# Kernel optimization log

Measured on AMD Instinct MI355X. Metric: run time of the kernel, lower is better.

Reference implementation:

```python
import jax, jax.numpy as jnp
import numpy as np

SEQ_LEN = 96
PRED_LEN = 16
HIDDEN = 64
FEAT = 7
BATCH = 512


def setup_inputs() -> dict:
    key = jax.random.key(0)
    ks = jax.random.split(key, 7)
    s = 1.0 / np.sqrt(HIDDEN)  # PyTorch LSTM/Linear default uniform init bound
    x = jax.random.normal(ks[0], (BATCH, SEQ_LEN, FEAT), jnp.float32)
    W_ih = jax.random.uniform(ks[1], (4 * HIDDEN, FEAT), jnp.float32, -s, s)
    W_hh = jax.random.uniform(ks[2], (4 * HIDDEN, HIDDEN), jnp.float32, -s, s)
    b_ih = jax.random.uniform(ks[3], (4 * HIDDEN,), jnp.float32, -s, s)
    b_hh = jax.random.uniform(ks[4], (4 * HIDDEN,), jnp.float32, -s, s)
    fc_W = jax.random.uniform(ks[5], (FEAT, HIDDEN), jnp.float32, -s, s)
    fc_b = jax.random.uniform(ks[6], (FEAT,), jnp.float32, -s, s)
    return {"x": x, "W_ih": W_ih, "W_hh": W_hh, "b_ih": b_ih, "b_hh": b_hh,
            "fc_W": fc_W, "fc_b": fc_b}


def _lstm_last(x, h, c, W_ih, W_hh, b):
    # Precompute input-to-gate projections for the whole window: [B, T, 4H]
    xg = jnp.einsum('bti,gi->btg', x, W_ih) + b

    def cell(carry, xg_t):
        h, c = carry
        gates = xg_t + h @ W_hh.T            # [B, 4H], PyTorch gate order i,f,g,o
        i, f, g, o = jnp.split(gates, 4, axis=-1)
        i = jax.nn.sigmoid(i)
        f = jax.nn.sigmoid(f)
        g = jnp.tanh(g)
        o = jax.nn.sigmoid(o)
        c = f * c + i * g
        h = o * jnp.tanh(c)
        return (h, c), None

    (h, c), _ = jax.lax.scan(cell, (h, c), jnp.swapaxes(xg, 0, 1))
    return h, c


def reference(x, W_ih, W_hh, b_ih, b_hh, fc_W, fc_b):
    B = x.shape[0]
    b = b_ih + b_hh
    h = jnp.zeros((B, HIDDEN), x.dtype)
    c = jnp.zeros((B, HIDDEN), x.dtype)
    outs = []
    for _ in range(PRED_LEN):
        h, c = _lstm_last(x, h, c, W_ih, W_hh, b)
        pred = h @ fc_W.T + fc_b             # [B, 7]
        outs.append(pred)
        x = jnp.concatenate([x[:, 1:, :], pred[:, None, :]], axis=1)
    return jnp.stack(outs, axis=1)           # [B, PRED_LEN, 7]
```

## Files before the change

### kernel.cpp

```cpp
#include <hip/hip_runtime.h>

#define SEQ_LEN 96
#define PRED_LEN 16
#define HIDDEN 64
#define FEAT 7
#define BATCH 512
#define TL (SEQ_LEN + PRED_LEN)
#define XSTR 8

typedef float v2f __attribute__((ext_vector_type(2)));

#define L2E 1.4426950408889634f

__device__ __forceinline__ float qp_xor1(float v) {
    return __int_as_float(__builtin_amdgcn_mov_dpp(__float_as_int(v), 0xB1, 0xF, 0xF, true));
}
__device__ __forceinline__ float qp_xor2(float v) {
    return __int_as_float(__builtin_amdgcn_mov_dpp(__float_as_int(v), 0x4E, 0xF, 0xF, true));
}
__device__ __forceinline__ float qp_rot1(float v) {
    return __int_as_float(__builtin_amdgcn_mov_dpp(__float_as_int(v), 0x39, 0xF, 0xF, true));
}
__device__ __forceinline__ float qp_rot3(float v) {
    return __int_as_float(__builtin_amdgcn_mov_dpp(__float_as_int(v), 0x93, 0xF, 0xF, true));
}

__device__ __forceinline__ v2f pk_mul(v2f a, v2f b) {
    v2f d;
    asm("v_pk_mul_f32 %0, %1, %2" : "=v"(d) : "v"(a), "v"(b));
    return d;
}
__device__ __forceinline__ void pk_fma(v2f& acc, v2f a, v2f b) {
    asm("v_pk_fma_f32 %0, %1, %2, %0" : "+v"(acc) : "v"(a), "v"(b));
}

__global__ __launch_bounds__(256)
__attribute__((amdgpu_waves_per_eu(2, 2)))
void lstm_ar_kernel(
    const float* __restrict__ x,
    const float* __restrict__ W_ih,
    const float* __restrict__ W_hh,
    const float* __restrict__ b_ih,
    const float* __restrict__ b_hh,
    const float* __restrict__ fc_W,
    const float* __restrict__ fc_b,
    float* __restrict__ out)
{
    __shared__ float xs[TL * XSTR];
    __shared__ float hb0[HIDDEN];
    __shared__ float hb1[HIDDEN];
    __shared__ float hscr[HIDDEN];
    __shared__ float fcw[FEAT * HIDDEN];
    __shared__ float fcb[FEAT];

    const int tid = threadIdx.x;
    const int b   = blockIdx.x;
    const int u   = tid >> 2;
    const int q   = tid & 3;

    v2f wh[4][8];
    #pragma unroll
    for (int k = 0; k < 4; ++k) {
        const int gate = (q + k) & 3;
        const float* wr = W_hh + ((gate << 6) + u) * HIDDEN + (q << 4);
        #pragma unroll
        for (int j = 0; j < 8; ++j) wh[k][j] = *(const v2f*)(wr + 2 * j);
    }
    v2f wx[4];
    #pragma unroll
    for (int k = 0; k < 4; ++k) {
        const int gate = (q + k) & 3;
        const int row  = (gate << 6) + u;
        const int c0 = (q << 1), c1 = c0 + 1;
        wx[k].x = W_ih[row * FEAT + c0];
        wx[k].y = (c1 < FEAT) ? W_ih[row * FEAT + c1]
                              : (b_ih[row] + b_hh[row]);
    }

    const float bk  = (q == 2) ? (-2.0f * L2E) : (-L2E);
    const float bm  = (q == 2) ? 2.0f : 1.0f;
    const float bbc = (q == 2) ? -1.0f : 0.0f;

    float* const sink = hscr + ((u + (q << 4)) & 63);
    float* const wa1 = (q == 0) ? (hb1 + u) : sink;
    float* const wa0 = (q == 0) ? (hb0 + u) : sink;

    const float4* const h40 = (const float4*)(hb0 + (q << 4));
    const float4* const h41 = (const float4*)(hb1 + (q << 4));
    const float* const xq = xs + (q << 1);

    for (int i = tid; i < TL * XSTR; i += 256) {
        int r = i >> 3, f = i & 7;
        float v = 1.0f;
        if (f < FEAT) v = (r < SEQ_LEN) ? x[b * SEQ_LEN * FEAT + r * FEAT + f] : 0.0f;
        xs[i] = v;
    }
    for (int i = tid; i < FEAT * HIDDEN; i += 256) fcw[i] = fc_W[i];
    if (tid < FEAT)   fcb[tid] = fc_b[tid];
    if (tid < HIDDEN) hb0[tid] = 0.0f;
    float c = 0.0f;
    __syncthreads();

    auto step = [&](v2f xv, int nrow, const float4* __restrict__ h4,
                    float* __restrict__ wa) -> v2f {
        v2f A0 = pk_mul(wx[0], xv);
        v2f A1 = pk_mul(wx[1], xv);
        v2f A2 = pk_mul(wx[2], xv);
        v2f A3 = pk_mul(wx[3], xv);

        #pragma unroll
        for (int j = 0; j < 4; ++j) {
            float4 hv = h4[j];
            v2f lo; lo.x = hv.x; lo.y = hv.y;
            v2f hi; hi.x = hv.z; hi.y = hv.w;
            pk_fma(A0, wh[0][2*j],   lo);
            pk_fma(A1, wh[1][2*j],   lo);
            pk_fma(A2, wh[2][2*j],   lo);
            pk_fma(A3, wh[3][2*j],   lo);
            pk_fma(A0, wh[0][2*j+1], hi);
            pk_fma(A1, wh[1][2*j+1], hi);
            pk_fma(A2, wh[2][2*j+1], hi);
            pk_fma(A3, wh[3][2*j+1], hi);
        }

        float r0 = A0.x + A0.y;
        float r1 = A1.x + A1.y;
        float r2 = A2.x + A2.y;
        float r3 = A3.x + A3.y;
        float sum = r0 + qp_rot1(r3);
        sum += qp_xor2(r2);
        sum += qp_rot3(r1);

        float e   = __builtin_amdgcn_exp2f(sum * bk);
        float rc  = __builtin_amdgcn_rcpf(1.0f + e);
        float a   = fmaf(bm, rc, bbc);

        float p1 = qp_xor1(a);
        float p2 = qp_xor2(a);
        float p3 = qp_xor2(p1);

        c = fmaf(p1, c, a * p2);
        float e2 = __builtin_amdgcn_exp2f(c * (-2.0f * L2E));
        float rr = __builtin_amdgcn_rcpf(1.0f + e2);
        float th = fmaf(2.0f, rr, -1.0f);
        *wa = p3 * th;

        v2f nxt = *(const v2f*)(xq + nrow * XSTR);
        __syncthreads();
        return nxt;
    };

    for (int k = 0; k < PRED_LEN; ++k) {
        v2f cur = *(const v2f*)(xq + k * XSTR);
        for (int t = 0; t < SEQ_LEN; t += 2) {
            cur = step(cur, k + t + 1, h40, wa1);
            cur = step(cur, k + t + 2, h41, wa0);
        }

        if (tid < FEAT) {
            float p0 = fcb[tid], p1 = 0.0f, p2 = 0.0f, p3 = 0.0f;
            const float4* hh = (const float4*)hb0;
            #pragma unroll
            for (int j = 0; j < 16; ++j) {
                float4 hv = hh[j];
                p0 = fmaf(fcw[tid * HIDDEN + 4 * j + 0], hv.x, p0);
                p1 = fmaf(fcw[tid * HIDDEN + 4 * j + 1], hv.y, p1);
                p2 = fmaf(fcw[tid * HIDDEN + 4 * j + 2], hv.z, p2);
                p3 = fmaf(fcw[tid * HIDDEN + 4 * j + 3], hv.w, p3);
            }
            float pred = (p0 + p1) + (p2 + p3);
            out[(b * PRED_LEN + k) * FEAT + tid] = pred;
            xs[(SEQ_LEN + k) * XSTR + tid] = pred;
        }
        __syncthreads();
    }
}

extern "C" void kernel_launch(void* const* d_in, const int* in_sizes, int n_in,
                              void* d_out, int out_size, void* d_ws, size_t ws_size,
                              hipStream_t stream) {
    const float* x    = (const float*)d_in[0];
    const float* W_ih = (const float*)d_in[1];
    const float* W_hh = (const float*)d_in[2];
    const float* b_ih = (const float*)d_in[3];
    const float* b_hh = (const float*)d_in[4];
    const float* fc_W = (const float*)d_in[5];
    const float* fc_b = (const float*)d_in[6];
    float* out = (float*)d_out;

    lstm_ar_kernel<<<BATCH, 256, 0, stream>>>(x, W_ih, W_hh, b_ih, b_hh, fc_W, fc_b, out);
}
```

Measured before the change: 556.3 us.

## Process two batch rows per block to interleave independent LSTM recurrences

Each block now runs two batch elements in lockstep with one set of register-resident weights. The two independent dependency chains are interleaved, so FMA, transcendental and DPP latency can overlap and the per-step barrier is shared across two rows. The grid is halved to 256 blocks and waves-per-EU is lowered to 1, which gives more registers but leaves fewer waves per CU and fewer blocks than before on a 256-CU part.

```diff
diff --git a/kernel.cpp b/kernel.cpp
--- a/kernel.cpp
+++ b/kernel.cpp
@@ -34,8 +34,10 @@
     asm("v_pk_fma_f32 %0, %1, %2, %0" : "+v"(acc) : "v"(a), "v"(b));
 }
 
+struct VV { v2f a, b; };
+
 __global__ __launch_bounds__(256)
-__attribute__((amdgpu_waves_per_eu(2, 2)))
+__attribute__((amdgpu_waves_per_eu(1, 1)))
 void lstm_ar_kernel(
     const float* __restrict__ x,
     const float* __restrict__ W_ih,
@@ -46,15 +48,17 @@
     const float* __restrict__ fc_b,
     float* __restrict__ out)
 {
-    __shared__ float xs[TL * XSTR];
-    __shared__ float hb0[HIDDEN];
-    __shared__ float hb1[HIDDEN];
+    __shared__ float xsA[TL * XSTR];
+    __shared__ float xsB[TL * XSTR];
+    __shared__ float hA0[HIDDEN], hA1[HIDDEN];
+    __shared__ float hB0[HIDDEN], hB1[HIDDEN];
     __shared__ float hscr[HIDDEN];
     __shared__ float fcw[FEAT * HIDDEN];
     __shared__ float fcb[FEAT];
 
     const int tid = threadIdx.x;
-    const int b   = blockIdx.x;
+    const int bA  = blockIdx.x * 2;
+    const int bB  = bA + 1;
     const int u   = tid >> 2;
     const int q   = tid & 3;
 
@@ -82,95 +86,125 @@
     const float bbc = (q == 2) ? -1.0f : 0.0f;
 
     float* const sink = hscr + ((u + (q << 4)) & 63);
-    float* const wa1 = (q == 0) ? (hb1 + u) : sink;
-    float* const wa0 = (q == 0) ? (hb0 + u) : sink;
-
-    const float4* const h40 = (const float4*)(hb0 + (q << 4));
-    const float4* const h41 = (const float4*)(hb1 + (q << 4));
-    const float* const xq = xs + (q << 1);
+    float* const waA1 = (q == 0) ? (hA1 + u) : sink;
+    float* const waA0 = (q == 0) ? (hA0 + u) : sink;
+    float* const waB1 = (q == 0) ? (hB1 + u) : sink;
+    float* const waB0 = (q == 0) ? (hB0 + u) : sink;
+
+    const float4* const hA40 = (const float4*)(hA0 + (q << 4));
+    const float4* const hA41 = (const float4*)(hA1 + (q << 4));
+    const float4* const hB40 = (const float4*)(hB0 + (q << 4));
+    const float4* const hB41 = (const float4*)(hB1 + (q << 4));
+    const float* const xqA = xsA + (q << 1);
+    const float* const xqB = xsB + (q << 1);
 
     for (int i = tid; i < TL * XSTR; i += 256) {
         int r = i >> 3, f = i & 7;
-        float v = 1.0f;
-        if (f < FEAT) v = (r < SEQ_LEN) ? x[b * SEQ_LEN * FEAT + r * FEAT + f] : 0.0f;
-        xs[i] = v;
+        float vA = 1.0f, vB = 1.0f;
+        if (f < FEAT) {
+            vA = (r < SEQ_LEN) ? x[bA * SEQ_LEN * FEAT + r * FEAT + f] : 0.0f;
+            vB = (r < SEQ_LEN) ? x[bB * SEQ_LEN * FEAT + r * FEAT + f] : 0.0f;
+        }
+        xsA[i] = vA;
+        xsB[i] = vB;
     }
     for (int i = tid; i < FEAT * HIDDEN; i += 256) fcw[i] = fc_W[i];
     if (tid < FEAT)   fcb[tid] = fc_b[tid];
-    if (tid < HIDDEN) hb0[tid] = 0.0f;
-    float c = 0.0f;
+    if (tid < HIDDEN) { hA0[tid] = 0.0f; hB0[tid] = 0.0f; }
+    float cA = 0.0f, cB = 0.0f;
     __syncthreads();
 
-    auto step = [&](v2f xv, int nrow, const float4* __restrict__ h4,
-                    float* __restrict__ wa) -> v2f {
-        v2f A0 = pk_mul(wx[0], xv);
-        v2f A1 = pk_mul(wx[1], xv);
-        v2f A2 = pk_mul(wx[2], xv);
-        v2f A3 = pk_mul(wx[3], xv);
+    auto step = [&](v2f xvA, v2f xvB, int nrow,
+                    const float4* __restrict__ h4A, const float4* __restrict__ h4B,
+                    float* __restrict__ wA, float* __restrict__ wB) -> VV {
+        v2f nA = *(const v2f*)(xqA + nrow * XSTR);
+        v2f nB = *(const v2f*)(xqB + nrow * XSTR);
+
+        v2f A0 = pk_mul(wx[0], xvA);  v2f B0 = pk_mul(wx[0], xvB);
+        v2f A1 = pk_mul(wx[1], xvA);  v2f B1 = pk_mul(wx[1], xvB);
+        v2f A2 = pk_mul(wx[2], xvA);  v2f B2 = pk_mul(wx[2], xvB);
+        v2f A3 = pk_mul(wx[3], xvA);  v2f B3 = pk_mul(wx[3], xvB);
 
         #pragma unroll
         for (int j = 0; j < 4; ++j) {
-            float4 hv = h4[j];
-            v2f lo; lo.x = hv.x; lo.y = hv.y;
-            v2f hi; hi.x = hv.z; hi.y = hv.w;
-            pk_fma(A0, wh[0][2*j],   lo);
-            pk_fma(A1, wh[1][2*j],   lo);
-            pk_fma(A2, wh[2][2*j],   lo);
-            pk_fma(A3, wh[3][2*j],   lo);
-            pk_fma(A0, wh[0][2*j+1], hi);
-            pk_fma(A1, wh[1][2*j+1], hi);
-            pk_fma(A2, wh[2][2*j+1], hi);
-            pk_fma(A3, wh[3][2*j+1], hi);
-        }
-
-        float r0 = A0.x + A0.y;
-        float r1 = A1.x + A1.y;
-        float r2 = A2.x + A2.y;
-        float r3 = A3.x + A3.y;
-        float sum = r0 + qp_rot1(r3);
-        sum += qp_xor2(r2);
-        sum += qp_rot3(r1);
-
-        float e   = __builtin_amdgcn_exp2f(sum * bk);
-        float rc  = __builtin_amdgcn_rcpf(1.0f + e);
-        float a   = fmaf(bm, rc, bbc);
-
-        float p1 = qp_xor1(a);
-        float p2 = qp_xor2(a);
-        float p3 = qp_xor2(p1);
-
-        c = fmaf(p1, c, a * p2);
-        float e2 = __builtin_amdgcn_exp2f(c * (-2.0f * L2E));
-        float rr = __builtin_amdgcn_rcpf(1.0f + e2);
-        float th = fmaf(2.0f, rr, -1.0f);
-        *wa = p3 * th;
-
-        v2f nxt = *(const v2f*)(xq + nrow * XSTR);
+            float4 hvA = h4A[j];
+            float4 hvB = h4B[j];
+            v2f alo; alo.x = hvA.x; alo.y = hvA.y;
+            v2f ahi; ahi.x = hvA.z; ahi.y = hvA.w;
+            v2f blo; blo.x = hvB.x; blo.y = hvB.y;
+            v2f bhi; bhi.x = hvB.z; bhi.y = hvB.w;
+            pk_fma(A0, wh[0][2*j],   alo);  pk_fma(B0, wh[0][2*j],   blo);
+            pk_fma(A1, wh[1][2*j],   alo);  pk_fma(B1, wh[1][2*j],   blo);
+            pk_fma(A2, wh[2][2*j],   alo);  pk_fma(B2, wh[2][2*j],   blo);
+            pk_fma(A3, wh[3][2*j],   alo);  pk_fma(B3, wh[3][2*j],   blo);
+            pk_fma(A0, wh[0][2*j+1], ahi);  pk_fma(B0, wh[0][2*j+1], bhi);
+            pk_fma(A1, wh[1][2*j+1], ahi);  pk_fma(B1, wh[1][2*j+1], bhi);
+            pk_fma(A2, wh[2][2*j+1], ahi);  pk_fma(B2, wh[2][2*j+1], bhi);
+            pk_fma(A3, wh[3][2*j+1], ahi);  pk_fma(B3, wh[3][2*j+1], bhi);
+        }
+
+        float a0 = A0.x + A0.y, b0 = B0.x + B0.y;
+        float a1 = A1.x + A1.y, b1 = B1.x + B1.y;
+        float a2 = A2.x + A2.y, b2 = B2.x + B2.y;
+        float a3 = A3.x + A3.y, b3 = B3.x + B3.y;
+        float sA = (a0 + qp_rot1(a3)) + (qp_xor2(a2) + qp_rot3(a1));
+        float sB = (b0 + qp_rot1(b3)) + (qp_xor2(b2) + qp_rot3(b1));
+
+        float eA  = __builtin_amdgcn_exp2f(sA * bk);
+        float eB  = __builtin_amdgcn_exp2f(sB * bk);
+        float rA  = __builtin_amdgcn_rcpf(1.0f + eA);
+        float rB  = __builtin_amdgcn_rcpf(1.0f + eB);
+        float aA  = fmaf(bm, rA, bbc);
+        float aB  = fmaf(bm, rB, bbc);
+
+        float pA1 = qp_xor1(aA);       float pB1 = qp_xor1(aB);
+        float pA2 = qp_xor2(aA);       float pB2 = qp_xor2(aB);
+        float pA3 = qp_xor2(pA1);      float pB3 = qp_xor2(pB1);
+
+        cA = fmaf(pA1, cA, aA * pA2);
+        cB = fmaf(pB1, cB, aB * pB2);
+        float e2A = __builtin_amdgcn_exp2f(cA * (-2.0f * L2E));
+        float e2B = __builtin_amdgcn_exp2f(cB * (-2.0f * L2E));
+        float rrA = __builtin_amdgcn_rcpf(1.0f + e2A);
+        float rrB = __builtin_amdgcn_rcpf(1.0f + e2B);
+        float thA = fmaf(2.0f, rrA, -1.0f);
+        float thB = fmaf(2.0f, rrB, -1.0f);
+        *wA = pA3 * thA;
+        *wB = pB3 * thB;
+
         __syncthreads();
-        return nxt;
+        VV r; r.a = nA; r.b = nB;
+        return r;
     };
 
     for (int k = 0; k < PRED_LEN; ++k) {
-        v2f cur = *(const v2f*)(xq + k * XSTR);
+        v2f curA = *(const v2f*)(xqA + k * XSTR);
+        v2f curB = *(const v2f*)(xqB + k * XSTR);
         for (int t = 0; t < SEQ_LEN; t += 2) {
-            cur = step(cur, k + t + 1, h40, wa1);
-            cur = step(cur, k + t + 2, h41, wa0);
-        }
-
-        if (tid < FEAT) {
-            float p0 = fcb[tid], p1 = 0.0f, p2 = 0.0f, p3 = 0.0f;
-            const float4* hh = (const float4*)hb0;
+            VV r1 = step(curA, curB, k + t + 1, hA40, hB40, waA1, waB1);
+            curA = r1.a; curB = r1.b;
+            VV r2 = step(curA, curB, k + t + 2, hA41, hB41, waA0, waB0);
+            curA = r2.a; curB = r2.b;
+        }
+
+        const int w = tid >> 6, l = tid & 63;
+        if (w < 2 && l < FEAT) {
+            const float* hb = (w == 0) ? hA0 : hB0;
+            float*      xst = (w == 0) ? xsA : xsB;
+            const int   bb  = (w == 0) ? bA  : bB;
+            float p0 = fcb[l], p1 = 0.0f, p2 = 0.0f, p3 = 0.0f;
+            const float4* hh = (const float4*)hb;
             #pragma unroll
             for (int j = 0; j < 16; ++j) {
                 float4 hv = hh[j];
-                p0 = fmaf(fcw[tid * HIDDEN + 4 * j + 0], hv.x, p0);
-                p1 = fmaf(fcw[tid * HIDDEN + 4 * j + 1], hv.y, p1);
-                p2 = fmaf(fcw[tid * HIDDEN + 4 * j + 2], hv.z, p2);
-                p3 = fmaf(fcw[tid * HIDDEN + 4 * j + 3], hv.w, p3);
+                p0 = fmaf(fcw[l * HIDDEN + 4 * j + 0], hv.x, p0);
+                p1 = fmaf(fcw[l * HIDDEN + 4 * j + 1], hv.y, p1);
+                p2 = fmaf(fcw[l * HIDDEN + 4 * j + 2], hv.z, p2);
+                p3 = fmaf(fcw[l * HIDDEN + 4 * j + 3], hv.w, p3);
             }
             float pred = (p0 + p1) + (p2 + p3);
-            out[(b * PRED_LEN + k) * FEAT + tid] = pred;
-            xs[(SEQ_LEN + k) * XSTR + tid] = pred;
+            out[(bb * PRED_LEN + k) * FEAT + l] = pred;
+            xst[(SEQ_LEN + k) * XSTR + l] = pred;
         }
         __syncthreads();
     }
@@ -188,5 +222,5 @@
     const float* fc_b = (const float*)d_in[6];
     float* out = (float*)d_out;
 
-    lstm_ar_kernel<<<BATCH, 256, 0, stream>>>(x, W_ih, W_hh, b_ih, b_hh, fc_W, fc_b, out);
-}
+    lstm_ar_kernel<<<BATCH / 2, 256, 0, stream>>>(x, W_ih, W_hh, b_ih, b_hh, fc_W, fc_b, out);
+}
```

Result: slower. 682.6 us (+22.7%).
